# Kernel tuning notes

Hardware: AMD Instinct MI355X
Metric: run time of the kernel (lower is better)

Reference implementation:

```python
import jax, jax.numpy as jnp
import numpy as np

N_NODES = 50000
N_EDGES = 800000
IN_CH = 128
HID = 256


def gcn_layer(x, src, dst, W, b, n_nodes):
    # x: [N, F_in] -> h: [N, F_out]
    h = x @ W
    # add self loops (PyG GCNConv default)
    loop = jnp.arange(n_nodes, dtype=src.dtype)
    src_f = jnp.concatenate([src, loop])
    dst_f = jnp.concatenate([dst, loop])
    # symmetric normalization: deg^{-1/2}[src] * deg^{-1/2}[dst]
    deg = jax.ops.segment_sum(jnp.ones_like(dst_f, dtype=h.dtype), dst_f, num_segments=n_nodes)
    dinv = jnp.where(deg > 0, jax.lax.rsqrt(deg), 0.0)
    norm = dinv[src_f] * dinv[dst_f]  # [E+N]
    msg = h[src_f] * norm[:, None]    # [E+N, F_out] gather
    out = jax.ops.segment_sum(msg, dst_f, num_segments=n_nodes)  # scatter-add
    return out + b


def setup_inputs() -> dict:
    key = jax.random.key(0)
    k1, k2, k3, k4 = jax.random.split(key, 4)
    x = jax.random.normal(k1, (N_NODES, IN_CH), dtype=jnp.float32)
    edge_index = jax.random.randint(k2, (2, N_EDGES), 0, N_NODES, dtype=jnp.int64)
    W1 = jax.random.normal(k3, (IN_CH, HID), dtype=jnp.float32) * (1.0 / np.sqrt(IN_CH))
    b1 = jnp.zeros((HID,), dtype=jnp.float32)
    W2 = jax.random.normal(k4, (HID, HID), dtype=jnp.float32) * (1.0 / np.sqrt(HID))
    b2 = jnp.zeros((HID,), dtype=jnp.float32)
    return {"x": x, "edge_index": edge_index, "W1": W1, "b1": b1, "W2": W2, "b2": b2}


def reference(x, edge_index, W1, b1, W2, b2):
    src, dst = edge_index[0], edge_index[1]
    h = gcn_layer(x, src, dst, W1, b1, N_NODES)
    h = jax.nn.relu(h)
    # dropout in eval mode (training=False) is identity
    out = gcn_layer(h, src, dst, W2, b2, N_NODES)
    return out
```

## Files before the change

kernel.cpp:

```cpp
#include <hip/hip_runtime.h>

constexpr int N = 50000;
constexpr int E = 800000;
constexpr int NPAD = 50048;
constexpr int NB = (N + 255) / 256;

typedef _Float16 half8 __attribute__((ext_vector_type(8)));
typedef _Float16 half4v __attribute__((ext_vector_type(4)));
typedef float float4v __attribute__((ext_vector_type(4)));

__global__ __launch_bounds__(256) void deg_kernel(const int* __restrict__ dst,
                                                  int* __restrict__ degI) {
    int e = blockIdx.x * 256 + threadIdx.x;
    if (e < E) atomicAdd(&degI[dst[e]], 1);
}

__global__ __launch_bounds__(256) void dinv_kernel(const int* __restrict__ degI,
                                                   float* __restrict__ dinv) {
    int v = blockIdx.x * 256 + threadIdx.x;
    if (v < N) dinv[v] = rsqrtf((float)degI[v] + 1.0f);
}

__global__ __launch_bounds__(256) void scan1_kernel(const int* __restrict__ degI,
                                                    int* __restrict__ incl,
                                                    int* __restrict__ blockSums) {
    __shared__ int s[256];
    int t = threadIdx.x;
    int i = blockIdx.x * 256 + t;
    int d = (i < N) ? degI[i] : 0;
    s[t] = d;
    __syncthreads();
    for (int off = 1; off < 256; off <<= 1) {
        int v = s[t];
        int u = (t >= off) ? s[t - off] : 0;
        __syncthreads();
        s[t] = v + u;
        __syncthreads();
    }
    if (i < N) incl[i] = s[t];
    if (t == 255) blockSums[blockIdx.x] = s[255];
}

__global__ __launch_bounds__(256) void scan2_kernel(int* __restrict__ blockSums) {
    __shared__ int s[256];
    int t = threadIdx.x;
    int v = (t < NB) ? blockSums[t] : 0;
    s[t] = v;
    __syncthreads();
    for (int off = 1; off < 256; off <<= 1) {
        int a = s[t];
        int u = (t >= off) ? s[t - off] : 0;
        __syncthreads();
        s[t] = a + u;
        __syncthreads();
    }
    if (t < NB) blockSums[t] = s[t] - v;
}

__global__ __launch_bounds__(256) void scan3_kernel(const int* __restrict__ degI,
                                                    const int* __restrict__ incl,
                                                    const int* __restrict__ blockSums,
                                                    int* __restrict__ rowptr,
                                                    int* __restrict__ cursor) {
    int i = blockIdx.x * 256 + threadIdx.x;
    if (i < N) {
        int e = blockSums[blockIdx.x] + incl[i] - degI[i];
        rowptr[i] = e;
        cursor[i] = e;
    }
    if (i == 0) rowptr[N] = E;
}

__global__ __launch_bounds__(256) void fill_kernel(const int* __restrict__ src,
                                                   const int* __restrict__ dst,
                                                   int* __restrict__ cursor,
                                                   int* __restrict__ eidx) {
    int e = blockIdx.x * 256 + threadIdx.x;
    if (e >= E) return;
    int d = dst[e];
    int pos = atomicAdd(&cursor[d], 1);
    eidx[pos] = src[e];
}

template <int K>
__global__ __launch_bounds__(256) void wt_kernel(const float* __restrict__ W,
                                                 _Float16* __restrict__ Wt) {
    int idx = blockIdx.x * 256 + threadIdx.x;
    int k = idx & (K - 1);
    int n = idx >> (K == 128 ? 7 : 8);
    Wt[idx] = (_Float16)W[(size_t)k * 256 + n];
}

__global__ __launch_bounds__(256) void prescale_kernel(const float4* __restrict__ x,
                                                       const float* __restrict__ dinv,
                                                       half4v* __restrict__ px) {
    int idx = blockIdx.x * 256 + threadIdx.x;
    if (idx >= N * 32) return;
    float dv = dinv[idx >> 5];
    float4 t = x[idx];
    half4v o;
    o[0] = (_Float16)(t.x * dv);
    o[1] = (_Float16)(t.y * dv);
    o[2] = (_Float16)(t.z * dv);
    o[3] = (_Float16)(t.w * dv);
    px[idx] = o;
}

template <int T>
__global__ __launch_bounds__(256) void aggregate_wide(
    const int* __restrict__ rowptr, const int* __restrict__ eidx,
    const half8* __restrict__ f, const float* __restrict__ dinv,
    half8* __restrict__ q) {
    constexpr int LPN = T / 8;
    constexpr int NPB = 256 / LPN;

    const int v = blockIdx.x * NPB + threadIdx.x / LPN;
    if (v >= N) return;
    const int lane = threadIdx.x % LPN;
    const size_t base = (size_t)v * LPN + lane;

    half8 s = f[base];
    float a[8];
#pragma unroll
    for (int j = 0; j < 8; ++j) a[j] = (float)s[j];

    int i = rowptr[v];
    const int end = rowptr[v + 1];
    for (; i + 8 <= end; i += 8) {
        int e0 = eidx[i + 0], e1 = eidx[i + 1], e2 = eidx[i + 2], e3 = eidx[i + 3];
        int e4 = eidx[i + 4], e5 = eidx[i + 5], e6 = eidx[i + 6], e7 = eidx[i + 7];
        half8 t0 = f[(size_t)e0 * LPN + lane];
        half8 t1 = f[(size_t)e1 * LPN + lane];
        half8 t2 = f[(size_t)e2 * LPN + lane];
        half8 t3 = f[(size_t)e3 * LPN + lane];
        half8 t4 = f[(size_t)e4 * LPN + lane];
        half8 t5 = f[(size_t)e5 * LPN + lane];
        half8 t6 = f[(size_t)e6 * LPN + lane];
        half8 t7 = f[(size_t)e7 * LPN + lane];
#pragma unroll
        for (int j = 0; j < 8; ++j) {
            a[j] += (((float)t0[j] + (float)t1[j]) + ((float)t2[j] + (float)t3[j])) +
                    (((float)t4[j] + (float)t5[j]) + ((float)t6[j] + (float)t7[j]));
        }
    }
    for (; i + 2 <= end; i += 2) {
        int e0 = eidx[i], e1 = eidx[i + 1];
        half8 t0 = f[(size_t)e0 * LPN + lane];
        half8 t1 = f[(size_t)e1 * LPN + lane];
#pragma unroll
        for (int j = 0; j < 8; ++j) a[j] += (float)t0[j] + (float)t1[j];
    }
    if (i < end) {
        half8 t0 = f[(size_t)eidx[i] * LPN + lane];
#pragma unroll
        for (int j = 0; j < 8; ++j) a[j] += (float)t0[j];
    }

    float dv = dinv[v];
    half8 o;
#pragma unroll
    for (int j = 0; j < 8; ++j) o[j] = (_Float16)(a[j] * dv);
    q[base] = o;
}

template <int K, bool FUSE1>
__global__ __launch_bounds__(256) void gemm_mfma(
    const _Float16* __restrict__ A, const _Float16* __restrict__ Wt,
    const float* __restrict__ bias, const float* __restrict__ dinv,
    void* __restrict__ outp) {
    constexpr int LSTR = K + 8;
    __shared__ _Float16 Bs[64 * LSTR];

    const int tid = threadIdx.x;
    const int wave = tid >> 6;
    const int lane = tid & 63;
    const int m = lane & 15;
    const int quad = lane >> 4;
    const int rbase = blockIdx.x * 64 + wave * 16;
    const int row = rbase + m;

    half8 af[K / 32];
    {
        const half8* Arow = (const half8*)(A + (size_t)row * K);
#pragma unroll
        for (int i = 0; i < K / 32; ++i) af[i] = Arow[i * 4 + quad];
    }

    for (int cc = 0; cc < 4; ++cc) {
        const int colbase = cc * 64;
        if (cc) __syncthreads();
        {
            int col = tid >> 2;
            int sub = tid & 3;
            const half8* srcb = (const half8*)(Wt + (size_t)(colbase + col) * K);
            half8* dstb = (half8*)&Bs[col * LSTR];
#pragma unroll
            for (int u = 0; u < K / 32; ++u) dstb[sub + u * 4] = srcb[sub + u * 4];
        }
        __syncthreads();

        float4v acc[4] = {};
#pragma unroll
        for (int k0 = 0; k0 < K; k0 += 32) {
            half8 a = af[k0 >> 5];
#pragma unroll
            for (int c = 0; c < 4; ++c) {
                half8 b = *(const half8*)&Bs[(c * 16 + m) * LSTR + k0 + quad * 8];
                acc[c] = __builtin_amdgcn_mfma_f32_16x16x32_f16(a, b, acc[c], 0, 0, 0);
            }
        }

#pragma unroll
        for (int c = 0; c < 4; ++c) {
            int col = colbase + c * 16 + m;
            float bcol = bias[col];
#pragma unroll
            for (int r = 0; r < 4; ++r) {
                int orow = rbase + quad * 4 + r;
                if (orow < N) {
                    float val = acc[c][r] + bcol;
                    if (FUSE1) {
                        val = fmaxf(val, 0.f) * dinv[orow];
                        ((_Float16*)outp)[(size_t)orow * 256 + col] = (_Float16)val;
                    } else {
                        ((float*)outp)[(size_t)orow * 256 + col] = val;
                    }
                }
            }
        }
    }
}

extern "C" void kernel_launch(void* const* d_in, const int* in_sizes, int n_in,
                              void* d_out, int out_size, void* d_ws, size_t ws_size,
                              hipStream_t stream) {
    const float* x  = (const float*)d_in[0];
    const int* edge = (const int*)d_in[1];
    const int* src  = edge;
    const int* dst  = edge + E;
    const float* W1 = (const float*)d_in[2];
    const float* b1 = (const float*)d_in[3];
    const float* W2 = (const float*)d_in[4];
    const float* b2 = (const float*)d_in[5];
    float* out = (float*)d_out;

    _Float16* bufA = (_Float16*)d_ws;
    _Float16* bufB = bufA + (size_t)NPAD * 256;
    float* dinv    = (float*)(bufB + (size_t)NPAD * 256);
    int* degI      = (int*)(dinv + N);
    int* rowptr    = degI + N;
    int* cursor    = rowptr + (N + 1);
    int* eidx      = cursor + N;
    _Float16* W1t  = (_Float16*)(eidx + E);
    _Float16* W2t  = W1t + 256 * 128;
    int* blockSums = (int*)(W2t + 256 * 256);

    hipMemsetAsync(degI, 0, N * sizeof(int), stream);
    deg_kernel<<<(E + 255) / 256, 256, 0, stream>>>(dst, degI);
    dinv_kernel<<<(N + 255) / 256, 256, 0, stream>>>(degI, dinv);
    scan1_kernel<<<NB, 256, 0, stream>>>(degI, cursor, blockSums);
    scan2_kernel<<<1, 256, 0, stream>>>(blockSums);
    scan3_kernel<<<NB, 256, 0, stream>>>(degI, cursor, blockSums, rowptr, cursor);
    fill_kernel<<<(E + 255) / 256, 256, 0, stream>>>(src, dst, cursor, eidx);

    wt_kernel<128><<<(256 * 128) / 256, 256, 0, stream>>>(W1, W1t);
    wt_kernel<256><<<(256 * 256) / 256, 256, 0, stream>>>(W2, W2t);

    prescale_kernel<<<(N * 32 + 255) / 256, 256, 0, stream>>>(
        (const float4*)x, dinv, (half4v*)bufA);
    aggregate_wide<128><<<(N + 15) / 16, 256, 0, stream>>>(
        rowptr, eidx, (const half8*)bufA, dinv, (half8*)bufB);
    gemm_mfma<128, true><<<NPAD / 64, 256, 0, stream>>>(
        bufB, W1t, b1, dinv, bufA);

    aggregate_wide<256><<<(N + 7) / 8, 256, 0, stream>>>(
        rowptr, eidx, (const half8*)bufA, dinv, (half8*)bufB);
    gemm_mfma<256, false><<<NPAD / 64, 256, 0, stream>>>(
        bufB, W2t, b2, dinv, out);
}
```

Before: 323.5 us.

## Fuse sparse aggregation into MFMA GEMM via shared-memory A tile

The gather-aggregate stage now writes its 64-row output tile straight into LDS, and the MFMA GEMM in the same kernel consumes it, so the intermediate feature matrix no longer makes a round trip through global memory. The W tile is loaded in 32-column chunks to keep LDS use within budget. The dinv computation is folded into the first scan kernel and the two weight-transpose kernels are merged, removing launches. The cost is that each fused block does both the latency-bound gather and the GEMM, which may lower occupancy and overlap compared with separate kernels.

```diff
diff --git a/kernel.cpp b/kernel.cpp
--- a/kernel.cpp
+++ b/kernel.cpp
@@ -15,19 +15,15 @@
     if (e < E) atomicAdd(&degI[dst[e]], 1);
 }
 
-__global__ __launch_bounds__(256) void dinv_kernel(const int* __restrict__ degI,
-                                                   float* __restrict__ dinv) {
-    int v = blockIdx.x * 256 + threadIdx.x;
-    if (v < N) dinv[v] = rsqrtf((float)degI[v] + 1.0f);
-}
-
 __global__ __launch_bounds__(256) void scan1_kernel(const int* __restrict__ degI,
                                                     int* __restrict__ incl,
-                                                    int* __restrict__ blockSums) {
+                                                    int* __restrict__ blockSums,
+                                                    float* __restrict__ dinv) {
     __shared__ int s[256];
     int t = threadIdx.x;
     int i = blockIdx.x * 256 + t;
     int d = (i < N) ? degI[i] : 0;
+    if (i < N) dinv[i] = rsqrtf((float)d + 1.0f);
     s[t] = d;
     __syncthreads();
     for (int off = 1; off < 256; off <<= 1) {
@@ -82,13 +78,21 @@
     eidx[pos] = src[e];
 }
 
-template <int K>
-__global__ __launch_bounds__(256) void wt_kernel(const float* __restrict__ W,
-                                                 _Float16* __restrict__ Wt) {
+__global__ __launch_bounds__(256) void wt_both_kernel(const float* __restrict__ W1,
+                                                      const float* __restrict__ W2,
+                                                      _Float16* __restrict__ W1t,
+                                                      _Float16* __restrict__ W2t) {
     int idx = blockIdx.x * 256 + threadIdx.x;
-    int k = idx & (K - 1);
-    int n = idx >> (K == 128 ? 7 : 8);
-    Wt[idx] = (_Float16)W[(size_t)k * 256 + n];
+    if (idx < 256 * 128) {
+        int k = idx & 127;
+        int n = idx >> 7;
+        W1t[idx] = (_Float16)W1[(size_t)k * 256 + n];
+    } else {
+        int j = idx - 256 * 128;
+        int k = j & 255;
+        int n = j >> 8;
+        W2t[j] = (_Float16)W2[(size_t)k * 256 + n];
+    }
 }
 
 __global__ __launch_bounds__(256) void prescale_kernel(const float4* __restrict__ x,
@@ -106,112 +110,116 @@
     px[idx] = o;
 }
 
-template <int T>
-__global__ __launch_bounds__(256) void aggregate_wide(
+template <int K, bool FUSE1>
+__global__ __launch_bounds__(256) void fused_agg_gemm(
     const int* __restrict__ rowptr, const int* __restrict__ eidx,
-    const half8* __restrict__ f, const float* __restrict__ dinv,
-    half8* __restrict__ q) {
-    constexpr int LPN = T / 8;
-    constexpr int NPB = 256 / LPN;
-
-    const int v = blockIdx.x * NPB + threadIdx.x / LPN;
-    if (v >= N) return;
-    const int lane = threadIdx.x % LPN;
-    const size_t base = (size_t)v * LPN + lane;
-
-    half8 s = f[base];
-    float a[8];
-#pragma unroll
-    for (int j = 0; j < 8; ++j) a[j] = (float)s[j];
-
-    int i = rowptr[v];
-    const int end = rowptr[v + 1];
-    for (; i + 8 <= end; i += 8) {
-        int e0 = eidx[i + 0], e1 = eidx[i + 1], e2 = eidx[i + 2], e3 = eidx[i + 3];
-        int e4 = eidx[i + 4], e5 = eidx[i + 5], e6 = eidx[i + 6], e7 = eidx[i + 7];
-        half8 t0 = f[(size_t)e0 * LPN + lane];
-        half8 t1 = f[(size_t)e1 * LPN + lane];
-        half8 t2 = f[(size_t)e2 * LPN + lane];
-        half8 t3 = f[(size_t)e3 * LPN + lane];
-        half8 t4 = f[(size_t)e4 * LPN + lane];
-        half8 t5 = f[(size_t)e5 * LPN + lane];
-        half8 t6 = f[(size_t)e6 * LPN + lane];
-        half8 t7 = f[(size_t)e7 * LPN + lane];
-#pragma unroll
-        for (int j = 0; j < 8; ++j) {
-            a[j] += (((float)t0[j] + (float)t1[j]) + ((float)t2[j] + (float)t3[j])) +
-                    (((float)t4[j] + (float)t5[j]) + ((float)t6[j] + (float)t7[j]));
-        }
-    }
-    for (; i + 2 <= end; i += 2) {
-        int e0 = eidx[i], e1 = eidx[i + 1];
-        half8 t0 = f[(size_t)e0 * LPN + lane];
-        half8 t1 = f[(size_t)e1 * LPN + lane];
-#pragma unroll
-        for (int j = 0; j < 8; ++j) a[j] += (float)t0[j] + (float)t1[j];
-    }
-    if (i < end) {
-        half8 t0 = f[(size_t)eidx[i] * LPN + lane];
-#pragma unroll
-        for (int j = 0; j < 8; ++j) a[j] += (float)t0[j];
-    }
-
-    float dv = dinv[v];
-    half8 o;
-#pragma unroll
-    for (int j = 0; j < 8; ++j) o[j] = (_Float16)(a[j] * dv);
-    q[base] = o;
-}
-
-template <int K, bool FUSE1>
-__global__ __launch_bounds__(256) void gemm_mfma(
-    const _Float16* __restrict__ A, const _Float16* __restrict__ Wt,
+    const half8* __restrict__ f, const _Float16* __restrict__ Wt,
     const float* __restrict__ bias, const float* __restrict__ dinv,
     void* __restrict__ outp) {
+    constexpr int LPN = K / 8;
+    constexpr int NPB = 256 / LPN;
     constexpr int LSTR = K + 8;
-    __shared__ _Float16 Bs[64 * LSTR];
+    __shared__ _Float16 As[64 * LSTR];
+    __shared__ _Float16 Bs[32 * LSTR];
 
     const int tid = threadIdx.x;
+    const int rbase0 = blockIdx.x * 64;
+
+    {
+        const int lane = tid % LPN;
+        const int nsub = tid / LPN;
+        for (int r = 0; r < 64; r += NPB) {
+            const int row = r + nsub;
+            const int v = rbase0 + row;
+            float a[8] = {0.f, 0.f, 0.f, 0.f, 0.f, 0.f, 0.f, 0.f};
+            if (v < N) {
+                half8 s = f[(size_t)v * LPN + lane];
+#pragma unroll
+                for (int j = 0; j < 8; ++j) a[j] = (float)s[j];
+                int i = rowptr[v];
+                const int end = rowptr[v + 1];
+                for (; i + 8 <= end; i += 8) {
+                    int e0 = eidx[i + 0], e1 = eidx[i + 1];
+                    int e2 = eidx[i + 2], e3 = eidx[i + 3];
+                    int e4 = eidx[i + 4], e5 = eidx[i + 5];
+                    int e6 = eidx[i + 6], e7 = eidx[i + 7];
+                    half8 t0 = f[(size_t)e0 * LPN + lane];
+                    half8 t1 = f[(size_t)e1 * LPN + lane];
+                    half8 t2 = f[(size_t)e2 * LPN + lane];
+                    half8 t3 = f[(size_t)e3 * LPN + lane];
+                    half8 t4 = f[(size_t)e4 * LPN + lane];
+                    half8 t5 = f[(size_t)e5 * LPN + lane];
+                    half8 t6 = f[(size_t)e6 * LPN + lane];
+                    half8 t7 = f[(size_t)e7 * LPN + lane];
+#pragma unroll
+                    for (int j = 0; j < 8; ++j) {
+                        a[j] += (((float)t0[j] + (float)t1[j]) +
+                                 ((float)t2[j] + (float)t3[j])) +
+                                (((float)t4[j] + (float)t5[j]) +
+                                 ((float)t6[j] + (float)t7[j]));
+                    }
+                }
+                for (; i + 2 <= end; i += 2) {
+                    int e0 = eidx[i], e1 = eidx[i + 1];
+                    half8 t0 = f[(size_t)e0 * LPN + lane];
+                    half8 t1 = f[(size_t)e1 * LPN + lane];
+#pragma unroll
+                    for (int j = 0; j < 8; ++j) a[j] += (float)t0[j] + (float)t1[j];
+                }
+                if (i < end) {
+                    half8 t0 = f[(size_t)eidx[i] * LPN + lane];
+#pragma unroll
+                    for (int j = 0; j < 8; ++j) a[j] += (float)t0[j];
+                }
+                float dv = dinv[v];
+#pragma unroll
+                for (int j = 0; j < 8; ++j) a[j] *= dv;
+            }
+            half8 o;
+#pragma unroll
+            for (int j = 0; j < 8; ++j) o[j] = (_Float16)a[j];
+            *(half8*)&As[row * LSTR + lane * 8] = o;
+        }
+    }
+    __syncthreads();
+
     const int wave = tid >> 6;
-    const int lane = tid & 63;
-    const int m = lane & 15;
-    const int quad = lane >> 4;
-    const int rbase = blockIdx.x * 64 + wave * 16;
-    const int row = rbase + m;
+    const int l64 = tid & 63;
+    const int m = l64 & 15;
+    const int quad = l64 >> 4;
+    const int rbase = rbase0 + wave * 16;
 
     half8 af[K / 32];
-    {
-        const half8* Arow = (const half8*)(A + (size_t)row * K);
-#pragma unroll
-        for (int i = 0; i < K / 32; ++i) af[i] = Arow[i * 4 + quad];
-    }
-
-    for (int cc = 0; cc < 4; ++cc) {
-        const int colbase = cc * 64;
+#pragma unroll
+    for (int i = 0; i < K / 32; ++i)
+        af[i] = *(const half8*)&As[(wave * 16 + m) * LSTR + i * 32 + quad * 8];
+
+    for (int cc = 0; cc < 8; ++cc) {
+        const int colbase = cc * 32;
         if (cc) __syncthreads();
         {
-            int col = tid >> 2;
-            int sub = tid & 3;
+            int col = tid >> 3;
+            int sub = tid & 7;
             const half8* srcb = (const half8*)(Wt + (size_t)(colbase + col) * K);
             half8* dstb = (half8*)&Bs[col * LSTR];
 #pragma unroll
-            for (int u = 0; u < K / 32; ++u) dstb[sub + u * 4] = srcb[sub + u * 4];
-        }
-        __syncthreads();
-
-        float4v acc[4] = {};
+            for (int u = 0; u < K / 64; ++u) dstb[sub + u * 8] = srcb[sub + u * 8];
+        }
+        __syncthreads();
+
+        float4v acc[2] = {};
 #pragma unroll
         for (int k0 = 0; k0 < K; k0 += 32) {
             half8 a = af[k0 >> 5];
 #pragma unroll
-            for (int c = 0; c < 4; ++c) {
+            for (int c = 0; c < 2; ++c) {
                 half8 b = *(const half8*)&Bs[(c * 16 + m) * LSTR + k0 + quad * 8];
                 acc[c] = __builtin_amdgcn_mfma_f32_16x16x32_f16(a, b, acc[c], 0, 0, 0);
             }
         }
 
 #pragma unroll
-        for (int c = 0; c < 4; ++c) {
+        for (int c = 0; c < 2; ++c) {
             int col = colbase + c * 16 + m;
             float bcol = bias[col];
 #pragma unroll
@@ -257,24 +265,19 @@
 
     hipMemsetAsync(degI, 0, N * sizeof(int), stream);
     deg_kernel<<<(E + 255) / 256, 256, 0, stream>>>(dst, degI);
-    dinv_kernel<<<(N + 255) / 256, 256, 0, stream>>>(degI, dinv);
-    scan1_kernel<<<NB, 256, 0, stream>>>(degI, cursor, blockSums);
+    scan1_kernel<<<NB, 256, 0, stream>>>(degI, cursor, blockSums, dinv);
     scan2_kernel<<<1, 256, 0, stream>>>(blockSums);
     scan3_kernel<<<NB, 256, 0, stream>>>(degI, cursor, blockSums, rowptr, cursor);
     fill_kernel<<<(E + 255) / 256, 256, 0, stream>>>(src, dst, cursor, eidx);
 
-    wt_kernel<128><<<(256 * 128) / 256, 256, 0, stream>>>(W1, W1t);
-    wt_kernel<256><<<(256 * 256) / 256, 256, 0, stream>>>(W2, W2t);
+    wt_both_kernel<<<(256 * 128 + 256 * 256) / 256, 256, 0, stream>>>(
+        W1, W2, W1t, W2t);
 
     prescale_kernel<<<(N * 32 + 255) / 256, 256, 0, stream>>>(
         (const float4*)x, dinv, (half4v*)bufA);
-    aggregate_wide<128><<<(N + 15) / 16, 256, 0, stream>>>(
-        rowptr, eidx, (const half8*)bufA, dinv, (half8*)bufB);
-    gemm_mfma<128, true><<<NPAD / 64, 256, 0, stream>>>(
-        bufB, W1t, b1, dinv, bufA);
-
-    aggregate_wide<256><<<(N + 7) / 8, 256, 0, stream>>>(
-        rowptr, eidx, (const half8*)bufA, dinv, (half8*)bufB);
-    gemm_mfma<256, false><<<NPAD / 64, 256, 0, stream>>>(
-        bufB, W2t, b2, dinv, out);
-}
+    fused_agg_gemm<128, true><<<NPAD / 64, 256, 0, stream>>>(
+        rowptr, eidx, (const half8*)bufA, W1t, b1, dinv, bufB);
+
+    fused_agg_gemm<256, false><<<NPAD / 64, 256, 0, stream>>>(
+        rowptr, eidx, (const half8*)bufB, W2t, b2, dinv, out);
+}
```

After: 342.8 us. +5.9%, slower.
